# Kernel tuning notes

Measured on AMD Instinct MI355X. Metric: run time of the kernel, lower is better.

The kernel has to match this reference:

```python
import jax, jax.numpy as jnp
import numpy as np
from jax import lax

K = 3
STRIDE = 1
PAD = 1
DIL = 1
EPS = 1e-5


def conv2d(x, w, b):
    y = lax.conv_general_dilated(
        x, w, (STRIDE, STRIDE), [(PAD, PAD), (PAD, PAD)],
        rhs_dilation=(DIL, DIL), dimension_numbers=('NCHW', 'OIHW', 'NCHW'))
    return y + b[None, :, None, None]


def deform_conv(x, offset, w):
    # x: [B,C,H,W], offset: [B,2*K2,Ho,Wo] (dy,dx interleaved per tap), w: [O,C,K,K]
    B, C, H, W = x.shape
    O = w.shape[0]
    K2 = K * K
    Ho, Wo = offset.shape[2], offset.shape[3]
    ky, kx = jnp.meshgrid(jnp.arange(K), jnp.arange(K), indexing='ij')
    # base sampling grid per kernel tap: [K2,Ho,Wo] (broadcast)
    by = (ky.reshape(K2, 1, 1) * DIL).astype(x.dtype) + (jnp.arange(Ho) * STRIDE - PAD).astype(x.dtype).reshape(1, Ho, 1)
    bx = (kx.reshape(K2, 1, 1) * DIL).astype(x.dtype) + (jnp.arange(Wo) * STRIDE - PAD).astype(x.dtype).reshape(1, 1, Wo)
    off = offset.reshape(B, K2, 2, Ho, Wo)
    py = by[None] + off[:, :, 0]  # [B,K2,Ho,Wo]
    px = bx[None] + off[:, :, 1]
    y0 = jnp.floor(py)
    x0 = jnp.floor(px)
    wy = py - y0
    wx = px - x0
    y0i = y0.astype(jnp.int32)
    x0i = x0.astype(jnp.int32)
    x_flat = x.reshape(B, C, H * W)

    def corner(yi, xi, cw):
        valid = ((yi >= 0) & (yi < H) & (xi >= 0) & (xi < W)).astype(x.dtype)
        idx = (jnp.clip(yi, 0, H - 1) * W + jnp.clip(xi, 0, W - 1)).reshape(B, -1)
        v = jax.vmap(lambda xb, ib: xb[:, ib])(x_flat, idx)  # [B,C,K2*Ho*Wo]
        return v * (cw * valid).reshape(B, 1, -1)

    val = (corner(y0i, x0i, (1 - wy) * (1 - wx))
           + corner(y0i, x0i + 1, (1 - wy) * wx)
           + corner(y0i + 1, x0i, wy * (1 - wx))
           + corner(y0i + 1, x0i + 1, wy * wx))  # [B,C,K2*Ho*Wo]
    samp = val.reshape(B, C, K2, Ho * Wo)
    out = jnp.einsum('bckp,ock->bop', samp, w.reshape(O, C, K2))
    return out.reshape(B, O, Ho, Wo)


def bn_gelu(x, gamma, beta):
    m = x.mean((0, 2, 3), keepdims=True)
    v = x.var((0, 2, 3), keepdims=True)
    xn = (x - m) / jnp.sqrt(v + EPS) * gamma[None, :, None, None] + beta[None, :, None, None]
    return jax.nn.gelu(xn, approximate=False)


def deform_block(x, w_off, b_off, w_def, gamma, beta):
    offset = conv2d(x, w_off, b_off)
    return bn_gelu(deform_conv(x, offset, w_def), gamma, beta)


def setup_inputs() -> dict:
    key = jax.random.key(0)
    ks = jax.random.split(key, 8)
    B, C, H, W = 4, 128, 112, 112
    fan = C * K * K
    x = jax.random.normal(ks[0], (B, C, H, W), jnp.float32)
    # offset conv weights: small random (original inits to 0; randomized to exercise sampling)
    w_off1 = jax.random.normal(ks[1], (2 * K * K, C, K, K), jnp.float32) * 0.01
    b_off1 = jnp.zeros((2 * K * K,), jnp.float32)
    w_def1 = jax.random.normal(ks[2], (C, C, K, K), jnp.float32) / np.sqrt(fan)
    gamma1 = jnp.ones((C,), jnp.float32)
    beta1 = jnp.zeros((C,), jnp.float32)
    w_off2 = jax.random.normal(ks[3], (2 * K * K, C, K, K), jnp.float32) * 0.01
    b_off2 = jnp.zeros((2 * K * K,), jnp.float32)
    w_def2 = jax.random.normal(ks[4], (C, C, K, K), jnp.float32) / np.sqrt(fan)
    gamma2 = jnp.ones((C,), jnp.float32)
    beta2 = jnp.zeros((C,), jnp.float32)
    return dict(x=x, w_off1=w_off1, b_off1=b_off1, w_def1=w_def1, gamma1=gamma1, beta1=beta1,
                w_off2=w_off2, b_off2=b_off2, w_def2=w_def2, gamma2=gamma2, beta2=beta2)


def reference(x, w_off1, b_off1, w_def1, gamma1, beta1,
              w_off2, b_off2, w_def2, gamma2, beta2):
    inp = x
    x = deform_block(x, w_off1, b_off1, w_def1, gamma1, beta1)
    x = deform_block(x, w_off2, b_off2, w_def2, gamma2, beta2)
    return x + inp
```

## Files before the change

### kernel.cpp

```cpp
#include <hip/hip_runtime.h>
#include <hip/hip_bf16.h>
#include <math.h>

#define HW 12544
#define CC 128
#define BB 4

typedef short bf16x8 __attribute__((ext_vector_type(8)));
typedef float f32x4 __attribute__((ext_vector_type(4)));

__device__ __forceinline__ float bf2f(unsigned int u) {
  union { unsigned int i; float f; } v; v.i = u << 16; return v.f;
}
__device__ __forceinline__ unsigned short f2bf(float f) {
  __hip_bfloat16 h = __float2bfloat16(f);
  return *reinterpret_cast<unsigned short*>(&h);
}
__device__ __forceinline__ float gelu(float v) {
  return 0.5f * v * (1.f + erff(v * 0.70710678118654752f));
}
__device__ __forceinline__ unsigned uc4(const uint4& v, int q) {
  return q == 0 ? v.x : q == 1 ? v.y : q == 2 ? v.z : v.w;
}

__global__ __launch_bounds__(256) void to_nhwc(const float* __restrict__ x,
                                               unsigned short* __restrict__ xh) {
  const int pt = blockIdx.x, ct = blockIdx.y, b = blockIdx.z;
  const int p0 = pt * 32, c0 = ct * 32;
  const int tid = threadIdx.x;
  __shared__ float ls[32][33];
  int col = tid & 31, r = tid >> 5;
#pragma unroll
  for (int i = 0; i < 4; i++) {
    int c = c0 + r + i * 8;
    ls[r + i * 8][col] = x[((size_t)(b * CC) + c) * HW + p0 + col];
  }
  __syncthreads();
  int px = tid >> 3, cq = (tid & 7) * 4;
  ushort4 v;
  v.x = f2bf(ls[cq + 0][px]);
  v.y = f2bf(ls[cq + 1][px]);
  v.z = f2bf(ls[cq + 2][px]);
  v.w = f2bf(ls[cq + 3][px]);
  *(ushort4*)&xh[((size_t)(b * HW) + p0 + px) * CC + c0 + cq] = v;
}

__global__ void pack_all(const float* __restrict__ wd1, const float* __restrict__ wo1,
                         const float* __restrict__ wd2, const float* __restrict__ wo2,
                         unsigned short* __restrict__ wpk1, unsigned short* __restrict__ wopk1,
                         unsigned short* __restrict__ wpk2, unsigned short* __restrict__ wopk2) {
  int i = blockIdx.x * 256 + threadIdx.x;
  if (i < 294912) {
    int ii = (i < 147456) ? i : i - 147456;
    const float* src = (i < 147456) ? wd1 : wd2;
    unsigned short* dst = (i < 147456) ? wpk1 : wpk2;
    int j = ii & 7, lane = (ii >> 3) & 63, ks = (ii >> 9) & 3, mo = (ii >> 11) & 7, k2 = ii >> 14;
    int o = mo * 16 + (lane & 15), c = ks * 32 + ((lane >> 4) << 3) + j;
    dst[ii] = f2bf(src[(o * CC + c) * 9 + k2]);
  } else {
    int ii = i - 294912;
    const float* src = (ii < 36864) ? wo1 : wo2;
    unsigned short* dst = (ii < 36864) ? wopk1 : wopk2;
    ii = (ii < 36864) ? ii : ii - 36864;
    int j = ii & 7, lane = (ii >> 3) & 63, ks = (ii >> 9) & 3, mo = (ii >> 11) & 1, k2 = ii >> 12;
    int o = mo * 16 + (lane & 15), c = ks * 32 + ((lane >> 4) << 3) + j;
    dst[ii] = (o < 18) ? f2bf(src[(o * CC + c) * 9 + k2]) : (unsigned short)0;
  }
}

__global__ __launch_bounds__(256) void offset_mfma(
    const unsigned short* __restrict__ xh, const unsigned short* __restrict__ wopk,
    const float* __restrict__ boff, float* __restrict__ offs2) {
  const int bid0 = blockIdx.x;
  const int bid = (bid0 & 7) * 98 + (bid0 >> 3);
  const int b = bid / 196;
  const int p0 = (bid % 196) * 64;
  const int tid = threadIdx.x;
  const int l = tid & 63, w = tid >> 6;
  const int hl = l & 15, ph = l >> 4;
  const int row = l & 15, grp = l >> 4;
  __shared__ unsigned short s_smp[2][8192];
  const unsigned short* xb = xh + (size_t)b * HW * CC + hl * 8;
  f32x4 acc[2];
  acc[0] = (f32x4){0.f, 0.f, 0.f, 0.f};
  acc[1] = (f32x4){0.f, 0.f, 0.f, 0.f};
  uint4 g2[4];
  bf16x8 af[2][4];

#define OISSUE(K2T)                                                            \
  {                                                                            \
    int ky = (K2T) / 3, kx = (K2T) % 3;                                        \
    _Pragma("unroll") for (int s = 0; s < 4; s++) {                            \
      int pxl = w * 16 + s * 4 + ph;                                           \
      int p = p0 + pxl;                                                        \
      int ho = p / 112, wo = p - ho * 112;                                     \
      int y = ho + ky - 1, x = wo + kx - 1;                                    \
      uint4 t = make_uint4(0u, 0u, 0u, 0u);                                    \
      if (((unsigned)y < 112u) & ((unsigned)x < 112u))                         \
        t = *(const uint4*)&xb[(size_t)(y * 112 + x) * CC];                    \
      g2[s] = t;                                                               \
    }                                                                          \
  }

#define OCOMMIT(BNBUF)                                                         \
  _Pragma("unroll") for (int s = 0; s < 4; s++) {                              \
    int pxl = w * 16 + s * 4 + ph;                                             \
    *(uint4*)((char*)&s_smp[BNBUF][0] +                                        \
              ((pxl * 256 + hl * 16) ^ ((pxl & 7) << 4))) = g2[s];             \
  }

#define OMFMA(BCBUF, ksB)                                                      \
  __builtin_amdgcn_s_setprio(1);                                               \
  _Pragma("unroll") for (int ks = ksB; ks < ksB + 2; ks++) {                   \
    int pxr = w * 16 + row;                                                    \
    bf16x8 bfr = *(const bf16x8*)((const char*)&s_smp[BCBUF][0] +              \
                 ((pxr * 256 + ks * 64 + grp * 16) ^ ((pxr & 7) << 4)));       \
    _Pragma("unroll") for (int m = 0; m < 2; m++)                              \
      acc[m] = __builtin_amdgcn_mfma_f32_16x16x32_bf16(af[m][ks], bfr, acc[m], 0, 0, 0); \
  }                                                                            \
  __builtin_amdgcn_s_setprio(0);

#define OLOADW(K2T)                                                            \
  {                                                                            \
    const unsigned short* wb = wopk + (size_t)(K2T) * 4096;                    \
    _Pragma("unroll") for (int m = 0; m < 2; m++)                              \
      _Pragma("unroll") for (int ks = 0; ks < 4; ks++)                         \
        af[m][ks] = *(const bf16x8*)&wb[(m * 4 + ks) * 512 + l * 8];           \
  }

#define OITER(K2T, BC, BN)                                                     \
  {                                                                            \
    if ((K2T) < 8) { OISSUE((K2T) + 1); }                                      \
    OMFMA(BC, 0);                                                              \
    if ((K2T) < 8) { OCOMMIT(BN); }                                            \
    OMFMA(BC, 2);                                                              \
    if ((K2T) < 8) { OLOADW((K2T) + 1); }                                      \
  }

  OISSUE(0); OCOMMIT(0); OLOADW(0);
  OITER(0, 0, 1) OITER(1, 1, 0) OITER(2, 0, 1) OITER(3, 1, 0) OITER(4, 0, 1)
  OITER(5, 1, 0) OITER(6, 0, 1) OITER(7, 1, 0) OITER(8, 0, 1)
#undef OISSUE
#undef OCOMMIT
#undef OMFMA
#undef OLOADW
#undef OITER

  int p = p0 + w * 16 + row;
  {
    float2 w0 = make_float2(acc[0][0] + boff[grp * 4 + 0], acc[0][1] + boff[grp * 4 + 1]);
    float2 w1 = make_float2(acc[0][2] + boff[grp * 4 + 2], acc[0][3] + boff[grp * 4 + 3]);
    *(float2*)&offs2[((size_t)(b * 9 + grp * 2) * HW + p) * 2] = w0;
    *(float2*)&offs2[((size_t)(b * 9 + grp * 2 + 1) * HW + p) * 2] = w1;
    if (grp == 0) {
      float2 w2 = make_float2(acc[1][0] + boff[16], acc[1][1] + boff[17]);
      *(float2*)&offs2[((size_t)(b * 9 + 8) * HW + p) * 2] = w2;
    }
  }
}

__global__ __launch_bounds__(256, 3) void deform_mfma(
    const unsigned short* __restrict__ xh, const float* __restrict__ offs2,
    const unsigned short* __restrict__ wpk, unsigned short* __restrict__ zh,
    float* __restrict__ part) {
  const int bid0 = blockIdx.x;
  const int bid = (bid0 & 7) * 98 + (bid0 >> 3);
  const int b = bid / 196;
  const int p0 = (bid % 196) * 64;
  const int tid = threadIdx.x;
  const int l = tid & 63, w = tid >> 6;
  const int hl = l & 15, ph = l >> 4;
  const int row = l & 15, grp = l >> 4;
  __shared__ unsigned short s_smp[2][8192];
  __shared__ uint4 s_coord[9][64];

  for (int e = tid; e < 576; e += 256) {
    int k2 = e >> 6, px = e & 63;
    int p = p0 + px;
    int ho = p / 112, wo = p - ho * 112;
    int ky = k2 / 3, kx = k2 - 3 * ky;
    float2 dv = *(const float2*)&offs2[((size_t)(b * 9 + k2) * HW + p) * 2];
    float py = (float)(ho + ky - 1) + dv.x;
    float pxf = (float)(wo + kx - 1) + dv.y;
    float y0f = floorf(py), x0f = floorf(pxf);
    float wy = py - y0f, wx = pxf - x0f;
    int y0 = (int)y0f, x0 = (int)x0f;
    int y1 = y0 + 1, x1 = x0 + 1;
    bool iy0 = ((unsigned)y0 < 112u), iy1 = ((unsigned)y1 < 112u);
    bool ix0 = ((unsigned)x0 < 112u), ix1 = ((unsigned)x1 < 112u);
    float v00 = (iy0 & ix0) ? (1.f - wy) * (1.f - wx) : 0.f;
    float v01 = (iy0 & ix1) ? (1.f - wy) * wx : 0.f;
    float v10 = (iy1 & ix0) ? wy * (1.f - wx) : 0.f;
    float v11 = (iy1 & ix1) ? wy * wx : 0.f;
    int y0c = min(max(y0, 0), 111), y1c = min(max(y1, 0), 111);
    int x0c = min(max(x0, 0), 111), x1c = min(max(x1, 0), 111);
    uint4 ce;
    ce.x = (unsigned)(y0c * 112 + x0c) | ((unsigned)(y0c * 112 + x1c) << 16);
    ce.y = (unsigned)(y1c * 112 + x0c) | ((unsigned)(y1c * 112 + x1c) << 16);
    ce.z = (unsigned)f2bf(v00) | ((unsigned)f2bf(v01) << 16);
    ce.w = (unsigned)f2bf(v10) | ((unsigned)f2bf(v11) << 16);
    s_coord[k2][px] = ce;
  }

  const unsigned short* xb = xh + (size_t)b * HW * CC + hl * 8;
  f32x4 acc[2][4];
#pragma unroll
  for (int m = 0; m < 2; m++)
#pragma unroll
    for (int n = 0; n < 4; n++) acc[m][n] = (f32x4){0.f, 0.f, 0.f, 0.f};
  uint4 g[4][4];
  uint2 wts[4];
  bf16x8 af[2][4];
  __syncthreads();

#define DISSUE(K2T)                                                            \
  _Pragma("unroll") for (int s = 0; s < 4; s++) {                              \
    int pxl = w * 16 + s * 4 + ph;                                             \
    uint4 cc = s_coord[K2T][pxl];                                              \
    wts[s] = make_uint2(cc.z, cc.w);                                           \
    g[s][0] = *(const uint4*)&xb[(size_t)(cc.x & 0xffffu) * CC];               \
    g[s][1] = *(const uint4*)&xb[(size_t)(cc.x >> 16) * CC];                   \
    g[s][2] = *(const uint4*)&xb[(size_t)(cc.y & 0xffffu) * CC];               \
    g[s][3] = *(const uint4*)&xb[(size_t)(cc.y >> 16) * CC];                   \
  }

#define DCOMMIT(BNBUF)                                                         \
  _Pragma("unroll") for (int s = 0; s < 4; s++) {                              \
    int pxl = w * 16 + s * 4 + ph;                                             \
    float w00 = bf2f(wts[s].x & 0xffffu), w01 = bf2f(wts[s].x >> 16);          \
    float w10 = bf2f(wts[s].y & 0xffffu), w11 = bf2f(wts[s].y >> 16);          \
    unsigned rr[4];                                                            \
    _Pragma("unroll") for (int q = 0; q < 4; q++) {                            \
      unsigned a0 = uc4(g[s][0], q), a1 = uc4(g[s][1], q);                     \
      unsigned a2 = uc4(g[s][2], q), a3 = uc4(g[s][3], q);                     \
      float elo = w00 * bf2f(a0 & 0xffffu) + w01 * bf2f(a1 & 0xffffu)          \
                + w10 * bf2f(a2 & 0xffffu) + w11 * bf2f(a3 & 0xffffu);         \
      float ehi = w00 * bf2f(a0 >> 16) + w01 * bf2f(a1 >> 16)                  \
                + w10 * bf2f(a2 >> 16) + w11 * bf2f(a3 >> 16);                 \
      rr[q] = (unsigned)f2bf(elo) | ((unsigned)f2bf(ehi) << 16);               \
    }                                                                          \
    *(uint4*)((char*)&s_smp[BNBUF][0] +                                        \
              ((pxl * 256 + hl * 16) ^ ((pxl & 7) << 4))) =                    \
        make_uint4(rr[0], rr[1], rr[2], rr[3]);                                \
  }

#define DMFMA(BCBUF, ksB)                                                      \
  __builtin_amdgcn_s_setprio(1);                                               \
  _Pragma("unroll") for (int ks = ksB; ks < ksB + 2; ks++) {                   \
    bf16x8 bfr[4];                                                             \
    _Pragma("unroll") for (int n = 0; n < 4; n++) {                            \
      int pxr = n * 16 + row;                                                  \
      bfr[n] = *(const bf16x8*)((const char*)&s_smp[BCBUF][0] +                \
               ((pxr * 256 + ks * 64 + grp * 16) ^ ((pxr & 7) << 4)));         \
    }                                                                          \
    _Pragma("unroll") for (int m = 0; m < 2; m++)                              \
      _Pragma("unroll") for (int n = 0; n < 4; n++)                            \
        acc[m][n] = __builtin_amdgcn_mfma_f32_16x16x32_bf16(af[m][ks], bfr[n], acc[m][n], 0, 0, 0); \
  }                                                                            \
  __builtin_amdgcn_s_setprio(0);

#define DLOADW(K2T)                                                            \
  {                                                                            \
    const unsigned short* wb = wpk + (size_t)((K2T) * 8 + w * 2) * 2048;       \
    _Pragma("unroll") for (int m = 0; m < 2; m++)                              \
      _Pragma("unroll") for (int ks = 0; ks < 4; ks++)                         \
        af[m][ks] = *(const bf16x8*)&wb[(m * 4 + ks) * 512 + l * 8];           \
  }

#define DITER(K2T, BC, BN)                                                     \
  {                                                                            \
    if ((K2T) < 8) { DISSUE((K2T) + 1); }                                      \
    DMFMA(BC, 0);                                                              \
    if ((K2T) < 8) { DCOMMIT(BN); }                                            \
    DMFMA(BC, 2);                                                              \
    if ((K2T) < 8) { DLOADW((K2T) + 1); __syncthreads(); }                     \
  }

  DISSUE(0); DCOMMIT(0); DLOADW(0);
  __syncthreads();
  DITER(0, 0, 1) DITER(1, 1, 0) DITER(2, 0, 1) DITER(3, 1, 0) DITER(4, 0, 1)
  DITER(5, 1, 0) DITER(6, 0, 1) DITER(7, 1, 0) DITER(8, 0, 1)
#undef DISSUE
#undef DCOMMIT
#undef DMFMA
#undef DLOADW
#undef DITER

#pragma unroll
  for (int m = 0; m < 2; m++)
#pragma unroll
    for (int n = 0; n < 4; n++) {
      int o = (w * 2 + m) * 16 + grp * 4;
      size_t px = (size_t)(b * HW) + p0 + n * 16 + row;
      unsigned lo = (unsigned)f2bf(acc[m][n][0]) | ((unsigned)f2bf(acc[m][n][1]) << 16);
      unsigned hi = (unsigned)f2bf(acc[m][n][2]) | ((unsigned)f2bf(acc[m][n][3]) << 16);
      *(uint2*)&zh[px * CC + o] = make_uint2(lo, hi);
    }

  float sv[8], qv[8];
#pragma unroll
  for (int m = 0; m < 2; m++)
#pragma unroll
    for (int r = 0; r < 4; r++) {
      float s = 0.f, q = 0.f;
#pragma unroll
      for (int n = 0; n < 4; n++) { float v = acc[m][n][r]; s += v; q += v * v; }
      sv[m * 4 + r] = s; qv[m * 4 + r] = q;
    }
#pragma unroll
  for (int d = 1; d < 16; d <<= 1)
#pragma unroll
    for (int i = 0; i < 8; i++) {
      sv[i] += __shfl_xor(sv[i], d);
      qv[i] += __shfl_xor(qv[i], d);
    }
  if (row == 0) {
#pragma unroll
    for (int m = 0; m < 2; m++)
#pragma unroll
      for (int r = 0; r < 4; r++) {
        int ch = (w * 2 + m) * 16 + grp * 4 + r;
        part[(size_t)ch * 784 + bid] = sv[m * 4 + r];
        part[(size_t)(128 + ch) * 784 + bid] = qv[m * 4 + r];
      }
  }
}

__global__ __launch_bounds__(256) void bn_fin(const float* __restrict__ part,
                                              const float* __restrict__ gamma,
                                              const float* __restrict__ beta,
                                              float* __restrict__ stats) {
  const int c = blockIdx.x, t = threadIdx.x;
  float s = 0.f, q = 0.f;
  for (int j = t; j < 784; j += 256) {
    s += part[(size_t)c * 784 + j];
    q += part[(size_t)(128 + c) * 784 + j];
  }
  __shared__ float ss[256], sq2[256];
  ss[t] = s; sq2[t] = q;
  __syncthreads();
  for (int d = 128; d > 0; d >>= 1) {
    if (t < d) { ss[t] += ss[t + d]; sq2[t] += sq2[t + d]; }
    __syncthreads();
  }
  if (t == 0) {
    float N = 50176.f;
    float m = ss[0] / N;
    float var = sq2[0] / N - m * m;
    stats[c] = m;
    stats[128 + c] = rsqrtf(var + 1e-5f) * gamma[c];
    stats[256 + c] = beta[c];
  }
}

__global__ __launch_bounds__(256) void bn_gelu_to_bf16(
    const unsigned short* __restrict__ zh, const float* __restrict__ stats,
    unsigned short* __restrict__ yh) {
  int i = blockIdx.x * 256 + threadIdx.x;
  int c0 = (i & 15) * 8;
  uint4 zv = ((const uint4*)zh)[i];
  f32x4 m0 = *(const f32x4*)&stats[c0], m1 = *(const f32x4*)&stats[c0 + 4];
  f32x4 r0 = *(const f32x4*)&stats[128 + c0], r1 = *(const f32x4*)&stats[128 + c0 + 4];
  f32x4 b0 = *(const f32x4*)&stats[256 + c0], b1 = *(const f32x4*)&stats[256 + c0 + 4];
  float v[8] = {bf2f(zv.x & 0xffffu), bf2f(zv.x >> 16), bf2f(zv.y & 0xffffu), bf2f(zv.y >> 16),
                bf2f(zv.z & 0xffffu), bf2f(zv.z >> 16), bf2f(zv.w & 0xffffu), bf2f(zv.w >> 16)};
  unsigned o[4];
#pragma unroll
  for (int j = 0; j < 4; j++) {
    float mj0 = (j < 2) ? m0[j * 2] : m1[j * 2 - 4], mj1 = (j < 2) ? m0[j * 2 + 1] : m1[j * 2 - 3];
    float rj0 = (j < 2) ? r0[j * 2] : r1[j * 2 - 4], rj1 = (j < 2) ? r0[j * 2 + 1] : r1[j * 2 - 3];
    float bj0 = (j < 2) ? b0[j * 2] : b1[j * 2 - 4], bj1 = (j < 2) ? b0[j * 2 + 1] : b1[j * 2 - 3];
    float e0 = gelu((v[j * 2] - mj0) * rj0 + bj0);
    float e1 = gelu((v[j * 2 + 1] - mj1) * rj1 + bj1);
    o[j] = (unsigned)f2bf(e0) | ((unsigned)f2bf(e1) << 16);
  }
  ((uint4*)yh)[i] = make_uint4(o[0], o[1], o[2], o[3]);
}

__global__ __launch_bounds__(256) void bn_gelu_final(
    const unsigned short* __restrict__ zh, const float* __restrict__ stats,
    const float* __restrict__ x, float* __restrict__ out) {
  const int pt = blockIdx.x, b = blockIdx.y;
  const int p0 = pt * 16;
  const int tid = threadIdx.x;
  __shared__ float ls[16][129];
  {
    int cq = tid & 15, r = tid >> 4;
    uint4 zv = *(const uint4*)&zh[((size_t)(b * HW) + p0 + r) * CC + cq * 8];
    float v[8] = {bf2f(zv.x & 0xffffu), bf2f(zv.x >> 16), bf2f(zv.y & 0xffffu), bf2f(zv.y >> 16),
                  bf2f(zv.z & 0xffffu), bf2f(zv.z >> 16), bf2f(zv.w & 0xffffu), bf2f(zv.w >> 16)};
    f32x4 m0 = *(const f32x4*)&stats[cq * 8], m1 = *(const f32x4*)&stats[cq * 8 + 4];
    f32x4 r0 = *(const f32x4*)&stats[128 + cq * 8], r1 = *(const f32x4*)&stats[128 + cq * 8 + 4];
    f32x4 b0 = *(const f32x4*)&stats[256 + cq * 8], b1 = *(const f32x4*)&stats[256 + cq * 8 + 4];
#pragma unroll
    for (int j = 0; j < 4; j++) {
      ls[r][cq * 8 + j] = gelu((v[j] - m0[j]) * r0[j] + b0[j]);
      ls[r][cq * 8 + 4 + j] = gelu((v[4 + j] - m1[j]) * r1[j] + b1[j]);
    }
  }
  __syncthreads();
  int c = tid & 127, half = tid >> 7;
  const float* xr = x + ((size_t)(b * CC) + c) * HW + p0 + half * 8;
  float* orow = out + ((size_t)(b * CC) + c) * HW + p0 + half * 8;
  float4 o1 = make_float4(ls[half * 8 + 0][c], ls[half * 8 + 1][c],
                          ls[half * 8 + 2][c], ls[half * 8 + 3][c]);
  float4 o2 = make_float4(ls[half * 8 + 4][c], ls[half * 8 + 5][c],
                          ls[half * 8 + 6][c], ls[half * 8 + 7][c]);
  float4 x1 = *(const float4*)&xr[0];
  float4 x2 = *(const float4*)&xr[4];
  o1.x += x1.x; o1.y += x1.y; o1.z += x1.z; o1.w += x1.w;
  o2.x += x2.x; o2.y += x2.y; o2.z += x2.z; o2.w += x2.w;
  *(float4*)&orow[0] = o1;
  *(float4*)&orow[4] = o2;
}

extern "C" void kernel_launch(void* const* d_in, const int* in_sizes, int n_in,
                              void* d_out, int out_size, void* d_ws, size_t ws_size,
                              hipStream_t stream) {
  const float* x = (const float*)d_in[0];
  const float* w_off1 = (const float*)d_in[1];
  const float* b_off1 = (const float*)d_in[2];
  const float* w_def1 = (const float*)d_in[3];
  const float* gamma1 = (const float*)d_in[4];
  const float* beta1 = (const float*)d_in[5];
  const float* w_off2 = (const float*)d_in[6];
  const float* b_off2 = (const float*)d_in[7];
  const float* w_def2 = (const float*)d_in[8];
  const float* gamma2 = (const float*)d_in[9];
  const float* beta2 = (const float*)d_in[10];
  float* out = (float*)d_out;

  char* ws = (char*)d_ws;
  unsigned short* xhb = (unsigned short*)ws;
  unsigned short* zhb = (unsigned short*)(ws + 12845056);
  float* offb = (float*)(ws + 25690112);
  unsigned short* wpk1 = (unsigned short*)(ws + 29302784);
  unsigned short* wpk2 = (unsigned short*)(ws + 29597696);
  unsigned short* wopk1 = (unsigned short*)(ws + 29892608);
  unsigned short* wopk2 = (unsigned short*)(ws + 29966336);
  float* partb = (float*)(ws + 30040064);
  float* statsb = (float*)(ws + 30842880);

  to_nhwc<<<dim3(392, 4, 4), 256, 0, stream>>>(x, xhb);
  pack_all<<<1440, 256, 0, stream>>>(w_def1, w_off1, w_def2, w_off2,
                                     wpk1, wopk1, wpk2, wopk2);

  offset_mfma<<<784, 256, 0, stream>>>(xhb, wopk1, b_off1, offb);
  deform_mfma<<<784, 256, 0, stream>>>(xhb, offb, wpk1, zhb, partb);
  bn_fin<<<128, 256, 0, stream>>>(partb, gamma1, beta1, statsb);
  bn_gelu_to_bf16<<<3136, 256, 0, stream>>>(zhb, statsb, xhb);

  offset_mfma<<<784, 256, 0, stream>>>(xhb, wopk2, b_off2, offb);
  deform_mfma<<<784, 256, 0, stream>>>(xhb, offb, wpk2, zhb, partb);
  bn_fin<<<128, 256, 0, stream>>>(partb, gamma2, beta2, statsb);
  bn_gelu_final<<<dim3(784, 4), 256, 0, stream>>>(zhb, statsb, x, out);
}
```

Before: 205.5 us.

## Fuse offset convolution into deformable conv kernel via shared-memory offsets

Merges the offset-prediction MFMA kernel into the deformable-conv kernel. Each block computes its 64 pixels' offsets into shared memory, then computes bilinear coordinates and weights inline during each tap's gather instead of precomputing a coordinate table. This removes a kernel launch and the global round trip of the offset tensor per block. It also splits the weight-fragment loads across the two MFMA halves and adds sched_barriers. The cost is more register pressure and inline address arithmetic in the gather path under the 3-blocks-per-CU bound, and an s_off read with no visible barrier after it is written.

Measured after the change: 283.4 us. 37.9% more time.

```diff
diff --git a/kernel.cpp b/kernel.cpp
--- a/kernel.cpp
+++ b/kernel.cpp
@@ -68,9 +68,10 @@
   }
 }
 
-__global__ __launch_bounds__(256) void offset_mfma(
+__global__ __launch_bounds__(256, 3) void deform_fused(
     const unsigned short* __restrict__ xh, const unsigned short* __restrict__ wopk,
-    const float* __restrict__ boff, float* __restrict__ offs2) {
+    const float* __restrict__ boff, const unsigned short* __restrict__ wpk,
+    unsigned short* __restrict__ zh, float* __restrict__ part) {
   const int bid0 = blockIdx.x;
   const int bid = (bid0 & 7) * 98 + (bid0 >> 3);
   const int b = bid / 196;
@@ -80,26 +81,35 @@
   const int hl = l & 15, ph = l >> 4;
   const int row = l & 15, grp = l >> 4;
   __shared__ unsigned short s_smp[2][8192];
+  __shared__ float s_off[64][20];
   const unsigned short* xb = xh + (size_t)b * HW * CC + hl * 8;
-  f32x4 acc[2];
-  acc[0] = (f32x4){0.f, 0.f, 0.f, 0.f};
-  acc[1] = (f32x4){0.f, 0.f, 0.f, 0.f};
-  uint4 g2[4];
-  bf16x8 af[2][4];
+
+  int hoA[4], woA[4];
+#pragma unroll
+  for (int s = 0; s < 4; s++) {
+    int p = p0 + w * 16 + s * 4 + ph;
+    hoA[s] = p / 112;
+    woA[s] = p - hoA[s] * 112;
+  }
+
+  {
+    f32x4 facc[2];
+    facc[0] = (f32x4){0.f, 0.f, 0.f, 0.f};
+    facc[1] = (f32x4){0.f, 0.f, 0.f, 0.f};
+    uint4 g2[4];
+    bf16x8 af[2][4];
 
 #define OISSUE(K2T)                                                            \
   {                                                                            \
-    int ky = (K2T) / 3, kx = (K2T) % 3;                                        \
+    const int ky = (K2T) / 3, kx = (K2T) % 3;                                  \
     _Pragma("unroll") for (int s = 0; s < 4; s++) {                            \
-      int pxl = w * 16 + s * 4 + ph;                                           \
-      int p = p0 + pxl;                                                        \
-      int ho = p / 112, wo = p - ho * 112;                                     \
-      int y = ho + ky - 1, x = wo + kx - 1;                                    \
+      int y = hoA[s] + ky - 1, x = woA[s] + kx - 1;                            \
       uint4 t = make_uint4(0u, 0u, 0u, 0u);                                    \
       if (((unsigned)y < 112u) & ((unsigned)x < 112u))                         \
         t = *(const uint4*)&xb[(size_t)(y * 112 + x) * CC];                    \
       g2[s] = t;                                                               \
     }                                                                          \
+    __builtin_amdgcn_sched_barrier(0);                                         \
   }
 
 #define OCOMMIT(BNBUF)                                                         \
@@ -116,7 +126,7 @@
     bf16x8 bfr = *(const bf16x8*)((const char*)&s_smp[BCBUF][0] +              \
                  ((pxr * 256 + ks * 64 + grp * 16) ^ ((pxr & 7) << 4)));       \
     _Pragma("unroll") for (int m = 0; m < 2; m++)                              \
-      acc[m] = __builtin_amdgcn_mfma_f32_16x16x32_bf16(af[m][ks], bfr, acc[m], 0, 0, 0); \
+      facc[m] = __builtin_amdgcn_mfma_f32_16x16x32_bf16(af[m][ks], bfr, facc[m], 0, 0, 0); \
   }                                                                            \
   __builtin_amdgcn_s_setprio(0);
 
@@ -137,72 +147,25 @@
     if ((K2T) < 8) { OLOADW((K2T) + 1); }                                      \
   }
 
-  OISSUE(0); OCOMMIT(0); OLOADW(0);
-  OITER(0, 0, 1) OITER(1, 1, 0) OITER(2, 0, 1) OITER(3, 1, 0) OITER(4, 0, 1)
-  OITER(5, 1, 0) OITER(6, 0, 1) OITER(7, 1, 0) OITER(8, 0, 1)
+    OISSUE(0); OCOMMIT(0); OLOADW(0);
+    OITER(0, 0, 1) OITER(1, 1, 0) OITER(2, 0, 1) OITER(3, 1, 0) OITER(4, 0, 1)
+    OITER(5, 1, 0) OITER(6, 0, 1) OITER(7, 1, 0) OITER(8, 0, 1)
 #undef OISSUE
 #undef OCOMMIT
 #undef OMFMA
 #undef OLOADW
 #undef OITER
 
-  int p = p0 + w * 16 + row;
-  {
-    float2 w0 = make_float2(acc[0][0] + boff[grp * 4 + 0], acc[0][1] + boff[grp * 4 + 1]);
-    float2 w1 = make_float2(acc[0][2] + boff[grp * 4 + 2], acc[0][3] + boff[grp * 4 + 3]);
-    *(float2*)&offs2[((size_t)(b * 9 + grp * 2) * HW + p) * 2] = w0;
-    *(float2*)&offs2[((size_t)(b * 9 + grp * 2 + 1) * HW + p) * 2] = w1;
+    int pxe = w * 16 + row;
+#pragma unroll
+    for (int r2 = 0; r2 < 4; r2++)
+      s_off[pxe][grp * 4 + r2] = facc[0][r2] + boff[grp * 4 + r2];
     if (grp == 0) {
-      float2 w2 = make_float2(acc[1][0] + boff[16], acc[1][1] + boff[17]);
-      *(float2*)&offs2[((size_t)(b * 9 + 8) * HW + p) * 2] = w2;
+      s_off[pxe][16] = facc[1][0] + boff[16];
+      s_off[pxe][17] = facc[1][1] + boff[17];
     }
   }
-}
-
-__global__ __launch_bounds__(256, 3) void deform_mfma(
-    const unsigned short* __restrict__ xh, const float* __restrict__ offs2,
-    const unsigned short* __restrict__ wpk, unsigned short* __restrict__ zh,
-    float* __restrict__ part) {
-  const int bid0 = blockIdx.x;
-  const int bid = (bid0 & 7) * 98 + (bid0 >> 3);
-  const int b = bid / 196;
-  const int p0 = (bid % 196) * 64;
-  const int tid = threadIdx.x;
-  const int l = tid & 63, w = tid >> 6;
-  const int hl = l & 15, ph = l >> 4;
-  const int row = l & 15, grp = l >> 4;
-  __shared__ unsigned short s_smp[2][8192];
-  __shared__ uint4 s_coord[9][64];
-
-  for (int e = tid; e < 576; e += 256) {
-    int k2 = e >> 6, px = e & 63;
-    int p = p0 + px;
-    int ho = p / 112, wo = p - ho * 112;
-    int ky = k2 / 3, kx = k2 - 3 * ky;
-    float2 dv = *(const float2*)&offs2[((size_t)(b * 9 + k2) * HW + p) * 2];
-    float py = (float)(ho + ky - 1) + dv.x;
-    float pxf = (float)(wo + kx - 1) + dv.y;
-    float y0f = floorf(py), x0f = floorf(pxf);
-    float wy = py - y0f, wx = pxf - x0f;
-    int y0 = (int)y0f, x0 = (int)x0f;
-    int y1 = y0 + 1, x1 = x0 + 1;
-    bool iy0 = ((unsigned)y0 < 112u), iy1 = ((unsigned)y1 < 112u);
-    bool ix0 = ((unsigned)x0 < 112u), ix1 = ((unsigned)x1 < 112u);
-    float v00 = (iy0 & ix0) ? (1.f - wy) * (1.f - wx) : 0.f;
-    float v01 = (iy0 & ix1) ? (1.f - wy) * wx : 0.f;
-    float v10 = (iy1 & ix0) ? wy * (1.f - wx) : 0.f;
-    float v11 = (iy1 & ix1) ? wy * wx : 0.f;
-    int y0c = min(max(y0, 0), 111), y1c = min(max(y1, 0), 111);
-    int x0c = min(max(x0, 0), 111), x1c = min(max(x1, 0), 111);
-    uint4 ce;
-    ce.x = (unsigned)(y0c * 112 + x0c) | ((unsigned)(y0c * 112 + x1c) << 16);
-    ce.y = (unsigned)(y1c * 112 + x0c) | ((unsigned)(y1c * 112 + x1c) << 16);
-    ce.z = (unsigned)f2bf(v00) | ((unsigned)f2bf(v01) << 16);
-    ce.w = (unsigned)f2bf(v10) | ((unsigned)f2bf(v11) << 16);
-    s_coord[k2][px] = ce;
-  }
-
-  const unsigned short* xb = xh + (size_t)b * HW * CC + hl * 8;
+
   f32x4 acc[2][4];
 #pragma unroll
   for (int m = 0; m < 2; m++)
@@ -211,17 +174,35 @@
   uint4 g[4][4];
   uint2 wts[4];
   bf16x8 af[2][4];
-  __syncthreads();
 
 #define DISSUE(K2T)                                                            \
-  _Pragma("unroll") for (int s = 0; s < 4; s++) {                              \
-    int pxl = w * 16 + s * 4 + ph;                                             \
-    uint4 cc = s_coord[K2T][pxl];                                              \
-    wts[s] = make_uint2(cc.z, cc.w);                                           \
-    g[s][0] = *(const uint4*)&xb[(size_t)(cc.x & 0xffffu) * CC];               \
-    g[s][1] = *(const uint4*)&xb[(size_t)(cc.x >> 16) * CC];                   \
-    g[s][2] = *(const uint4*)&xb[(size_t)(cc.y & 0xffffu) * CC];               \
-    g[s][3] = *(const uint4*)&xb[(size_t)(cc.y >> 16) * CC];                   \
+  {                                                                            \
+    const int ky = (K2T) / 3, kx = (K2T) % 3;                                  \
+    _Pragma("unroll") for (int s = 0; s < 4; s++) {                            \
+      int pxl = w * 16 + s * 4 + ph;                                           \
+      float2 dv = *(const float2*)&s_off[pxl][2 * (K2T)];                      \
+      float py = (float)(hoA[s] + ky - 1) + dv.x;                              \
+      float pxf = (float)(woA[s] + kx - 1) + dv.y;                             \
+      float y0f = floorf(py), x0f = floorf(pxf);                               \
+      float wy = py - y0f, wx2 = pxf - x0f;                                    \
+      int y0 = (int)y0f, x0 = (int)x0f;                                        \
+      int y1 = y0 + 1, x1 = x0 + 1;                                            \
+      bool iy0 = ((unsigned)y0 < 112u), iy1 = ((unsigned)y1 < 112u);           \
+      bool ix0 = ((unsigned)x0 < 112u), ix1 = ((unsigned)x1 < 112u);           \
+      float v00 = (iy0 & ix0) ? (1.f - wy) * (1.f - wx2) : 0.f;                \
+      float v01 = (iy0 & ix1) ? (1.f - wy) * wx2 : 0.f;                        \
+      float v10 = (iy1 & ix0) ? wy * (1.f - wx2) : 0.f;                        \
+      float v11 = (iy1 & ix1) ? wy * wx2 : 0.f;                                \
+      wts[s] = make_uint2((unsigned)f2bf(v00) | ((unsigned)f2bf(v01) << 16),   \
+                          (unsigned)f2bf(v10) | ((unsigned)f2bf(v11) << 16));  \
+      int y0c = min(max(y0, 0), 111), y1c = min(max(y1, 0), 111);              \
+      int x0c = min(max(x0, 0), 111), x1c = min(max(x1, 0), 111);              \
+      g[s][0] = *(const uint4*)&xb[(size_t)(y0c * 112 + x0c) * CC];            \
+      g[s][1] = *(const uint4*)&xb[(size_t)(y0c * 112 + x1c) * CC];            \
+      g[s][2] = *(const uint4*)&xb[(size_t)(y1c * 112 + x0c) * CC];            \
+      g[s][3] = *(const uint4*)&xb[(size_t)(y1c * 112 + x1c) * CC];            \
+    }                                                                          \
+    __builtin_amdgcn_sched_barrier(0);                                         \
   }
 
 #define DCOMMIT(BNBUF)                                                         \
@@ -259,11 +240,19 @@
   }                                                                            \
   __builtin_amdgcn_s_setprio(0);
 
-#define DLOADW(K2T)                                                            \
+#define DLOADW_A(K2T)                                                          \
   {                                                                            \
     const unsigned short* wb = wpk + (size_t)((K2T) * 8 + w * 2) * 2048;       \
     _Pragma("unroll") for (int m = 0; m < 2; m++)                              \
-      _Pragma("unroll") for (int ks = 0; ks < 4; ks++)                         \
+      _Pragma("unroll") for (int ks = 0; ks < 2; ks++)                         \
+        af[m][ks] = *(const bf16x8*)&wb[(m * 4 + ks) * 512 + l * 8];           \
+  }
+
+#define DLOADW_B(K2T)                                                          \
+  {                                                                            \
+    const unsigned short* wb = wpk + (size_t)((K2T) * 8 + w * 2) * 2048;       \
+    _Pragma("unroll") for (int m = 0; m < 2; m++)                              \
+      _Pragma("unroll") for (int ks = 2; ks < 4; ks++)                         \
         af[m][ks] = *(const bf16x8*)&wb[(m * 4 + ks) * 512 + l * 8];           \
   }
 
@@ -271,19 +260,20 @@
   {                                                                            \
     if ((K2T) < 8) { DISSUE((K2T) + 1); }                                      \
     DMFMA(BC, 0);                                                              \
-    if ((K2T) < 8) { DCOMMIT(BN); }                                            \
+    if ((K2T) < 8) { DLOADW_A((K2T) + 1); DCOMMIT(BN); }                       \
     DMFMA(BC, 2);                                                              \
-    if ((K2T) < 8) { DLOADW((K2T) + 1); __syncthreads(); }                     \
-  }
-
-  DISSUE(0); DCOMMIT(0); DLOADW(0);
+    if ((K2T) < 8) { DLOADW_B((K2T) + 1); __syncthreads(); }                   \
+  }
+
+  DISSUE(0); DCOMMIT(0); DLOADW_A(0); DLOADW_B(0);
   __syncthreads();
   DITER(0, 0, 1) DITER(1, 1, 0) DITER(2, 0, 1) DITER(3, 1, 0) DITER(4, 0, 1)
   DITER(5, 1, 0) DITER(6, 0, 1) DITER(7, 1, 0) DITER(8, 0, 1)
 #undef DISSUE
 #undef DCOMMIT
 #undef DMFMA
-#undef DLOADW
+#undef DLOADW_A
+#undef DLOADW_B
 #undef DITER
 
 #pragma unroll
@@ -301,11 +291,11 @@
 #pragma unroll
   for (int m = 0; m < 2; m++)
 #pragma unroll
-    for (int r = 0; r < 4; r++) {
+    for (int r2 = 0; r2 < 4; r2++) {
       float s = 0.f, q = 0.f;
 #pragma unroll
-      for (int n = 0; n < 4; n++) { float v = acc[m][n][r]; s += v; q += v * v; }
-      sv[m * 4 + r] = s; qv[m * 4 + r] = q;
+      for (int n = 0; n < 4; n++) { float v = acc[m][n][r2]; s += v; q += v * v; }
+      sv[m * 4 + r2] = s; qv[m * 4 + r2] = q;
     }
 #pragma unroll
   for (int d = 1; d < 16; d <<= 1)
@@ -318,10 +308,10 @@
 #pragma unroll
     for (int m = 0; m < 2; m++)
 #pragma unroll
-      for (int r = 0; r < 4; r++) {
-        int ch = (w * 2 + m) * 16 + grp * 4 + r;
-        part[(size_t)ch * 784 + bid] = sv[m * 4 + r];
-        part[(size_t)(128 + ch) * 784 + bid] = qv[m * 4 + r];
+      for (int r2 = 0; r2 < 4; r2++) {
+        int ch = (w * 2 + m) * 16 + grp * 4 + r2;
+        part[(size_t)ch * 784 + bid] = sv[m * 4 + r2];
+        part[(size_t)(128 + ch) * 784 + bid] = qv[m * 4 + r2];
       }
   }
 }
@@ -433,25 +423,22 @@
   char* ws = (char*)d_ws;
   unsigned short* xhb = (unsigned short*)ws;
   unsigned short* zhb = (unsigned short*)(ws + 12845056);
-  float* offb = (float*)(ws + 25690112);
-  unsigned short* wpk1 = (unsigned short*)(ws + 29302784);
-  unsigned short* wpk2 = (unsigned short*)(ws + 29597696);
-  unsigned short* wopk1 = (unsigned short*)(ws + 29892608);
-  unsigned short* wopk2 = (unsigned short*)(ws + 29966336);
-  float* partb = (float*)(ws + 30040064);
-  float* statsb = (float*)(ws + 30842880);
+  unsigned short* wpk1 = (unsigned short*)(ws + 25690112);
+  unsigned short* wpk2 = (unsigned short*)(ws + 25985024);
+  unsigned short* wopk1 = (unsigned short*)(ws + 26279936);
+  unsigned short* wopk2 = (unsigned short*)(ws + 26353664);
+  float* partb = (float*)(ws + 26427392);
+  float* statsb = (float*)(ws + 27230208);
 
   to_nhwc<<<dim3(392, 4, 4), 256, 0, stream>>>(x, xhb);
   pack_all<<<1440, 256, 0, stream>>>(w_def1, w_off1, w_def2, w_off2,
                                      wpk1, wopk1, wpk2, wopk2);
 
-  offset_mfma<<<784, 256, 0, stream>>>(xhb, wopk1, b_off1, offb);
-  deform_mfma<<<784, 256, 0, stream>>>(xhb, offb, wpk1, zhb, partb);
+  deform_fused<<<784, 256, 0, stream>>>(xhb, wopk1, b_off1, wpk1, zhb, partb);
   bn_fin<<<128, 256, 0, stream>>>(partb, gamma1, beta1, statsb);
   bn_gelu_to_bf16<<<3136, 256, 0, stream>>>(zhb, statsb, xhb);
 
-  offset_mfma<<<784, 256, 0, stream>>>(xhb, wopk2, b_off2, offb);
-  deform_mfma<<<784, 256, 0, stream>>>(xhb, offb, wpk2, zhb, partb);
+  deform_fused<<<784, 256, 0, stream>>>(xhb, wopk2, b_off2, wpk2, zhb, partb);
   bn_fin<<<128, 256, 0, stream>>>(partb, gamma2, beta2, statsb);
   bn_gelu_final<<<dim3(784, 4), 256, 0, stream>>>(zhb, statsb, x, out);
 }
```

## Cut register pressure in offset and deform MFMA kernels to raise occupancy

Applied to the files above, without the earlier changes.

Weight fragments are no longer prefetched into registers a step ahead. They are loaded straight from global memory (L1/L2) inside each MFMA step, which frees the af register array. The deform kernel's sampling coordinates are packed into a 16-bit base index plus dx/dy flags, the bilinear weights are read from shared memory at commit time instead of being held in registers, and launch bounds go from 3 to 4 blocks per CU. The offset kernel hoists the per-pixel row/column division out of the tap loop. In exchange, weight loads now sit on the MFMA critical path and their latency may not be hidden.

Measured after the change: 621.2 us. 3.02x slower.

```diff
diff --git a/kernel.cpp b/kernel.cpp
--- a/kernel.cpp
+++ b/kernel.cpp
@@ -81,20 +81,25 @@
   const int row = l & 15, grp = l >> 4;
   __shared__ unsigned short s_smp[2][8192];
   const unsigned short* xb = xh + (size_t)b * HW * CC + hl * 8;
+  const unsigned short* wlane = wopk + l * 8;
   f32x4 acc[2];
   acc[0] = (f32x4){0.f, 0.f, 0.f, 0.f};
   acc[1] = (f32x4){0.f, 0.f, 0.f, 0.f};
   uint4 g2[4];
-  bf16x8 af[2][4];
+
+  int hoA[4], woA[4];
+#pragma unroll
+  for (int s = 0; s < 4; s++) {
+    int p = p0 + w * 16 + s * 4 + ph;
+    hoA[s] = p / 112;
+    woA[s] = p - hoA[s] * 112;
+  }
 
 #define OISSUE(K2T)                                                            \
   {                                                                            \
-    int ky = (K2T) / 3, kx = (K2T) % 3;                                        \
+    const int ky = (K2T) / 3, kx = (K2T) % 3;                                  \
     _Pragma("unroll") for (int s = 0; s < 4; s++) {                            \
-      int pxl = w * 16 + s * 4 + ph;                                           \
-      int p = p0 + pxl;                                                        \
-      int ho = p / 112, wo = p - ho * 112;                                     \
-      int y = ho + ky - 1, x = wo + kx - 1;                                    \
+      int y = hoA[s] + ky - 1, x = woA[s] + kx - 1;                            \
       uint4 t = make_uint4(0u, 0u, 0u, 0u);                                    \
       if (((unsigned)y < 112u) & ((unsigned)x < 112u))                         \
         t = *(const uint4*)&xb[(size_t)(y * 112 + x) * CC];                    \
@@ -109,41 +114,33 @@
               ((pxl * 256 + hl * 16) ^ ((pxl & 7) << 4))) = g2[s];             \
   }
 
-#define OMFMA(BCBUF, ksB)                                                      \
+#define OMFMA(K2T, BCBUF, ksB)                                                 \
   __builtin_amdgcn_s_setprio(1);                                               \
   _Pragma("unroll") for (int ks = ksB; ks < ksB + 2; ks++) {                   \
     int pxr = w * 16 + row;                                                    \
     bf16x8 bfr = *(const bf16x8*)((const char*)&s_smp[BCBUF][0] +              \
                  ((pxr * 256 + ks * 64 + grp * 16) ^ ((pxr & 7) << 4)));       \
-    _Pragma("unroll") for (int m = 0; m < 2; m++)                              \
-      acc[m] = __builtin_amdgcn_mfma_f32_16x16x32_bf16(af[m][ks], bfr, acc[m], 0, 0, 0); \
+    _Pragma("unroll") for (int m = 0; m < 2; m++) {                            \
+      bf16x8 af = *(const bf16x8*)&wlane[((size_t)(K2T) * 4096) + (m * 4 + ks) * 512]; \
+      acc[m] = __builtin_amdgcn_mfma_f32_16x16x32_bf16(af, bfr, acc[m], 0, 0, 0); \
+    }                                                                          \
   }                                                                            \
   __builtin_amdgcn_s_setprio(0);
-
-#define OLOADW(K2T)                                                            \
-  {                                                                            \
-    const unsigned short* wb = wopk + (size_t)(K2T) * 4096;                    \
-    _Pragma("unroll") for (int m = 0; m < 2; m++)                              \
-      _Pragma("unroll") for (int ks = 0; ks < 4; ks++)                         \
-        af[m][ks] = *(const bf16x8*)&wb[(m * 4 + ks) * 512 + l * 8];           \
-  }
 
 #define OITER(K2T, BC, BN)                                                     \
   {                                                                            \
     if ((K2T) < 8) { OISSUE((K2T) + 1); }                                      \
-    OMFMA(BC, 0);                                                              \
+    OMFMA(K2T, BC, 0);                                                         \
     if ((K2T) < 8) { OCOMMIT(BN); }                                            \
-    OMFMA(BC, 2);                                                              \
-    if ((K2T) < 8) { OLOADW((K2T) + 1); }                                      \
-  }
-
-  OISSUE(0); OCOMMIT(0); OLOADW(0);
+    OMFMA(K2T, BC, 2);                                                         \
+  }
+
+  OISSUE(0); OCOMMIT(0);
   OITER(0, 0, 1) OITER(1, 1, 0) OITER(2, 0, 1) OITER(3, 1, 0) OITER(4, 0, 1)
   OITER(5, 1, 0) OITER(6, 0, 1) OITER(7, 1, 0) OITER(8, 0, 1)
 #undef OISSUE
 #undef OCOMMIT
 #undef OMFMA
-#undef OLOADW
 #undef OITER
 
   int p = p0 + w * 16 + row;
@@ -159,7 +156,7 @@
   }
 }
 
-__global__ __launch_bounds__(256, 3) void deform_mfma(
+__global__ __launch_bounds__(256, 4) void deform_mfma(
     const unsigned short* __restrict__ xh, const float* __restrict__ offs2,
     const unsigned short* __restrict__ wpk, unsigned short* __restrict__ zh,
     float* __restrict__ part) {
@@ -172,7 +169,8 @@
   const int hl = l & 15, ph = l >> 4;
   const int row = l & 15, grp = l >> 4;
   __shared__ unsigned short s_smp[2][8192];
-  __shared__ uint4 s_coord[9][64];
+  __shared__ unsigned short s_cidx[9][64];
+  __shared__ uint2 s_cwts[9][64];
 
   for (int e = tid; e < 576; e += 256) {
     int k2 = e >> 6, px = e & 63;
@@ -194,41 +192,46 @@
     float v11 = (iy1 & ix1) ? wy * wx : 0.f;
     int y0c = min(max(y0, 0), 111), y1c = min(max(y1, 0), 111);
     int x0c = min(max(x0, 0), 111), x1c = min(max(x1, 0), 111);
-    uint4 ce;
-    ce.x = (unsigned)(y0c * 112 + x0c) | ((unsigned)(y0c * 112 + x1c) << 16);
-    ce.y = (unsigned)(y1c * 112 + x0c) | ((unsigned)(y1c * 112 + x1c) << 16);
-    ce.z = (unsigned)f2bf(v00) | ((unsigned)f2bf(v01) << 16);
-    ce.w = (unsigned)f2bf(v10) | ((unsigned)f2bf(v11) << 16);
-    s_coord[k2][px] = ce;
+    unsigned idx0 = (unsigned)(y0c * 112 + x0c);
+    unsigned dx = (unsigned)(x1c - x0c);
+    unsigned dy = (unsigned)(y1c - y0c);
+    s_cidx[k2][px] = (unsigned short)(idx0 | (dx << 14) | (dy << 15));
+    s_cwts[k2][px] = make_uint2((unsigned)f2bf(v00) | ((unsigned)f2bf(v01) << 16),
+                                (unsigned)f2bf(v10) | ((unsigned)f2bf(v11) << 16));
   }
 
   const unsigned short* xb = xh + (size_t)b * HW * CC + hl * 8;
+  const unsigned short* wlane = wpk + (size_t)(w * 2) * 2048 + l * 8;
   f32x4 acc[2][4];
 #pragma unroll
   for (int m = 0; m < 2; m++)
 #pragma unroll
     for (int n = 0; n < 4; n++) acc[m][n] = (f32x4){0.f, 0.f, 0.f, 0.f};
   uint4 g[4][4];
-  uint2 wts[4];
-  bf16x8 af[2][4];
   __syncthreads();
 
 #define DISSUE(K2T)                                                            \
   _Pragma("unroll") for (int s = 0; s < 4; s++) {                              \
     int pxl = w * 16 + s * 4 + ph;                                             \
-    uint4 cc = s_coord[K2T][pxl];                                              \
-    wts[s] = make_uint2(cc.z, cc.w);                                           \
-    g[s][0] = *(const uint4*)&xb[(size_t)(cc.x & 0xffffu) * CC];               \
-    g[s][1] = *(const uint4*)&xb[(size_t)(cc.x >> 16) * CC];                   \
-    g[s][2] = *(const uint4*)&xb[(size_t)(cc.y & 0xffffu) * CC];               \
-    g[s][3] = *(const uint4*)&xb[(size_t)(cc.y >> 16) * CC];                   \
-  }
-
-#define DCOMMIT(BNBUF)                                                         \
+    unsigned cc = s_cidx[K2T][pxl];                                            \
+    unsigned i0 = cc & 0x3fffu;                                                \
+    unsigned dxs = (cc >> 14) & 1u, dys = cc >> 15;                            \
+    const unsigned short* a0 = &xb[(size_t)i0 * CC];                           \
+    const unsigned short* a1 = a0 + dxs * CC;                                  \
+    const unsigned short* a2 = a0 + dys * (112 * CC);                          \
+    const unsigned short* a3 = a2 + dxs * CC;                                  \
+    g[s][0] = *(const uint4*)a0;                                               \
+    g[s][1] = *(const uint4*)a1;                                               \
+    g[s][2] = *(const uint4*)a2;                                               \
+    g[s][3] = *(const uint4*)a3;                                               \
+  }
+
+#define DCOMMIT(K2T, BNBUF)                                                    \
   _Pragma("unroll") for (int s = 0; s < 4; s++) {                              \
     int pxl = w * 16 + s * 4 + ph;                                             \
-    float w00 = bf2f(wts[s].x & 0xffffu), w01 = bf2f(wts[s].x >> 16);          \
-    float w10 = bf2f(wts[s].y & 0xffffu), w11 = bf2f(wts[s].y >> 16);          \
+    uint2 wp = s_cwts[K2T][pxl];                                               \
+    float w00 = bf2f(wp.x & 0xffffu), w01 = bf2f(wp.x >> 16);                  \
+    float w10 = bf2f(wp.y & 0xffffu), w11 = bf2f(wp.y >> 16);                  \
     unsigned rr[4];                                                            \
     _Pragma("unroll") for (int q = 0; q < 4; q++) {                            \
       unsigned a0 = uc4(g[s][0], q), a1 = uc4(g[s][1], q);                     \
@@ -244,7 +247,7 @@
         make_uint4(rr[0], rr[1], rr[2], rr[3]);                                \
   }
 
-#define DMFMA(BCBUF, ksB)                                                      \
+#define DMFMA(K2T, BCBUF, ksB)                                                 \
   __builtin_amdgcn_s_setprio(1);                                               \
   _Pragma("unroll") for (int ks = ksB; ks < ksB + 2; ks++) {                   \
     bf16x8 bfr[4];                                                             \
@@ -253,37 +256,30 @@
       bfr[n] = *(const bf16x8*)((const char*)&s_smp[BCBUF][0] +                \
                ((pxr * 256 + ks * 64 + grp * 16) ^ ((pxr & 7) << 4)));         \
     }                                                                          \
-    _Pragma("unroll") for (int m = 0; m < 2; m++)                              \
+    _Pragma("unroll") for (int m = 0; m < 2; m++) {                            \
+      bf16x8 af = *(const bf16x8*)&wlane[(size_t)(K2T) * 16384 + (m * 4 + ks) * 512]; \
       _Pragma("unroll") for (int n = 0; n < 4; n++)                            \
-        acc[m][n] = __builtin_amdgcn_mfma_f32_16x16x32_bf16(af[m][ks], bfr[n], acc[m][n], 0, 0, 0); \
+        acc[m][n] = __builtin_amdgcn_mfma_f32_16x16x32_bf16(af, bfr[n], acc[m][n], 0, 0, 0); \
+    }                                                                          \
   }                                                                            \
   __builtin_amdgcn_s_setprio(0);
-
-#define DLOADW(K2T)                                                            \
-  {                                                                            \
-    const unsigned short* wb = wpk + (size_t)((K2T) * 8 + w * 2) * 2048;       \
-    _Pragma("unroll") for (int m = 0; m < 2; m++)                              \
-      _Pragma("unroll") for (int ks = 0; ks < 4; ks++)                         \
-        af[m][ks] = *(const bf16x8*)&wb[(m * 4 + ks) * 512 + l * 8];           \
-  }
 
 #define DITER(K2T, BC, BN)                                                     \
   {                                                                            \
     if ((K2T) < 8) { DISSUE((K2T) + 1); }                                      \
-    DMFMA(BC, 0);                                                              \
-    if ((K2T) < 8) { DCOMMIT(BN); }                                            \
-    DMFMA(BC, 2);                                                              \
-    if ((K2T) < 8) { DLOADW((K2T) + 1); __syncthreads(); }                     \
-  }
-
-  DISSUE(0); DCOMMIT(0); DLOADW(0);
+    DMFMA(K2T, BC, 0);                                                         \
+    if ((K2T) < 8) { DCOMMIT((K2T) + 1, BN); }                                 \
+    DMFMA(K2T, BC, 2);                                                         \
+    if ((K2T) < 8) { __syncthreads(); }                                        \
+  }
+
+  DISSUE(0); DCOMMIT(0, 0);
   __syncthreads();
   DITER(0, 0, 1) DITER(1, 1, 0) DITER(2, 0, 1) DITER(3, 1, 0) DITER(4, 0, 1)
   DITER(5, 1, 0) DITER(6, 0, 1) DITER(7, 1, 0) DITER(8, 0, 1)
 #undef DISSUE
 #undef DCOMMIT
 #undef DMFMA
-#undef DLOADW
 #undef DITER
 
 #pragma unroll
@@ -301,11 +297,11 @@
 #pragma unroll
   for (int m = 0; m < 2; m++)
 #pragma unroll
-    for (int r = 0; r < 4; r++) {
+    for (int r2 = 0; r2 < 4; r2++) {
       float s = 0.f, q = 0.f;
 #pragma unroll
-      for (int n = 0; n < 4; n++) { float v = acc[m][n][r]; s += v; q += v * v; }
-      sv[m * 4 + r] = s; qv[m * 4 + r] = q;
+      for (int n = 0; n < 4; n++) { float v = acc[m][n][r2]; s += v; q += v * v; }
+      sv[m * 4 + r2] = s; qv[m * 4 + r2] = q;
     }
 #pragma unroll
   for (int d = 1; d < 16; d <<= 1)
@@ -318,10 +314,10 @@
 #pragma unroll
     for (int m = 0; m < 2; m++)
 #pragma unroll
-      for (int r = 0; r < 4; r++) {
-        int ch = (w * 2 + m) * 16 + grp * 4 + r;
-        part[(size_t)ch * 784 + bid] = sv[m * 4 + r];
-        part[(size_t)(128 + ch) * 784 + bid] = qv[m * 4 + r];
+      for (int r2 = 0; r2 < 4; r2++) {
+        int ch = (w * 2 + m) * 16 + grp * 4 + r2;
+        part[(size_t)ch * 784 + bid] = sv[m * 4 + r2];
+        part[(size_t)(128 + ch) * 784 + bid] = qv[m * 4 + r2];
       }
   }
 }
```
